# Optimization experiments

Measured on AMD Instinct MI355X. Metric: run time of the kernel, lower is better.

Reference implementation:

```python
import jax, jax.numpy as jnp
import numpy as np

GAMMA = 0.99      # discount_factor
LAM = 0.95        # gae_decay
CLIP = 0.2        # clipping_param
LOG_2PI = float(np.log(2.0 * np.pi))

B, T, A = 512, 2048, 16


def setup_inputs() -> dict:
    key = jax.random.key(0)
    ks = jax.random.split(key, 8)
    rewards = jax.random.normal(ks[0], (B, T), dtype=jnp.float32)
    critic_out = jax.random.normal(ks[1], (B, T + 1), dtype=jnp.float32)
    mu = jax.random.normal(ks[2], (B, T, A), dtype=jnp.float32)
    sigma = jax.random.uniform(ks[3], (B, T, A), dtype=jnp.float32) * 0.5 + 0.5
    old_mu = jax.random.normal(ks[4], (B, T, A), dtype=jnp.float32)
    old_sigma = jax.random.uniform(ks[5], (B, T, A), dtype=jnp.float32) * 0.5 + 0.5
    actions = jax.random.normal(ks[6], (B, T, A), dtype=jnp.float32)
    dones = jax.random.randint(ks[7], (B, T), 0, 2, dtype=jnp.int32)
    return {"rewards": rewards, "critic_out": critic_out, "mu": mu, "sigma": sigma,
            "old_mu": old_mu, "old_sigma": old_sigma, "actions": actions, "dones": dones}


def _normal_log_prob(x, mu, sigma):
    return -jnp.log(sigma) - 0.5 * LOG_2PI - 0.5 * jnp.square((x - mu) / sigma)


def _gae(rewards, dones_f, critic_out):
    # td_residuals: rewards + gamma * V[1:] - V[:-1]   -> [B, T]
    td = rewards + GAMMA * critic_out[:, 1:] - critic_out[:, :-1]
    b, t = rewards.shape
    # Reversed recurrence: adv[t] = td[t] + gamma*lam*(1 - done[t+1]) * adv[t+1],
    # for t = T-2 .. 0; adv[T-1] stays 0 (matches original loop bounds).
    xs = (jnp.flip(td[:, : t - 1], axis=1).T,        # [T-1, B]
          jnp.flip(dones_f[:, 1:], axis=1).T)        # [T-1, B]

    def step(carry, x):
        td_t, d_t = x
        adv = td_t + GAMMA * LAM * (1.0 - d_t) * carry
        return adv, adv

    _, advs = jax.lax.scan(step, jnp.zeros((b,), rewards.dtype), xs)
    advs = jnp.flip(advs, axis=0).T                  # [B, T-1]
    return jnp.concatenate([advs, jnp.zeros((b, 1), rewards.dtype)], axis=1)


def reference(rewards, critic_out, mu, sigma, old_mu, old_sigma, actions, dones):
    dones_f = dones.astype(rewards.dtype)
    advantages = _gae(rewards, dones_f, critic_out)          # [B, T]
    lp = _normal_log_prob(actions, mu, sigma)                # [B, T, A]
    old_lp = _normal_log_prob(actions, old_mu, old_sigma)    # [B, T, A]
    ratio = jnp.exp(lp - old_lp)
    clipped = jnp.minimum(jnp.maximum(ratio, 1.0 + CLIP), 1.0 - CLIP)
    adv = advantages[..., None]                              # broadcast over action dim
    obj = jnp.minimum(adv * ratio, adv * clipped)
    entropy = jnp.log(sigma) + 0.5 + 0.5 * LOG_2PI           # Normal entropy, [B, T, A]
    return jnp.mean(obj) + entropy
```

## Files before the change

### kernel.cpp

```cpp
#include <hip/hip_runtime.h>
#include <math.h>

#define BB 512
#define TT 2048
#define AA 16
#define NTOT (512LL * 2048LL * 16LL)
#define GAMMA 0.99f
#define GLAM  0.9405f
#define ENTC  1.4189385332046727f

#define NB2 2048

__global__ __launch_bounds__(256) void gae_kernel(
    const float* __restrict__ rewards, const float* __restrict__ vout,
    const int* __restrict__ dones, float* __restrict__ adv)
{
    const int b   = blockIdx.x;
    const int tid = threadIdx.x;
    const float* rw = rewards + (size_t)b * TT;
    const float* V  = vout    + (size_t)b * (TT + 1);
    const int*   dn = dones   + (size_t)b * TT;
    float*       av = adv     + (size_t)b * TT;

    float ak[8], bk[8];
    float SA = 1.f, SB = 0.f;
    #pragma unroll
    for (int k = 0; k < 8; ++k) {
        int u = tid * 8 + k;
        float au, bu;
        if (u == 0) { au = 0.f; bu = 0.f; }
        else {
            int t = TT - 1 - u;
            bu = rw[t] + GAMMA * V[t + 1] - V[t];
            au = GLAM * (1.f - (float)dn[t + 1]);
        }
        ak[k] = au; bk[k] = bu;
        SB = au * SB + bu;
        SA = au * SA;
    }

    const int lane = tid & 63;
    const int wave = tid >> 6;

    #pragma unroll
    for (int off = 1; off < 64; off <<= 1) {
        float pA = __shfl_up(SA, off, 64);
        float pB = __shfl_up(SB, off, 64);
        if (lane >= off) { SB = SA * pB + SB; SA = SA * pA; }
    }

    __shared__ float wA[4], wB[4];
    if (lane == 63) { wA[wave] = SA; wB[wave] = SB; }
    __syncthreads();

    float PA = 1.f, PB = 0.f;
    for (int w = 0; w < wave; ++w) {
        float aw = wA[w], bw = wB[w];
        PB = aw * PB + bw;
        PA = aw * PA;
    }

    float EA = __shfl_up(SA, 1, 64);
    float EB = __shfl_up(SB, 1, 64);
    if (lane == 0) { EA = 1.f; EB = 0.f; }

    float x = EA * PB + EB;
    #pragma unroll
    for (int k = 0; k < 8; ++k) {
        x = ak[k] * x + bk[k];
        int u = tid * 8 + k;
        av[TT - 1 - u] = x;
    }
}

__device__ __forceinline__ float obj1(float x, float m, float s,
                                      float om, float os, float ad)
{
    float rs  = __builtin_amdgcn_rcpf(s);
    float ros = __builtin_amdgcn_rcpf(os);
    float z   = (x - m) * rs;
    float zo  = (x - om) * ros;
    float d   = 0.5f * (zo * zo - z * z);
    float ratio = os * rs * __expf(d);
    return fminf(ad * ratio, ad * 0.8f);
}

__global__ __launch_bounds__(256) void obj_kernel(
    const float* __restrict__ mu, const float* __restrict__ sigma,
    const float* __restrict__ old_mu, const float* __restrict__ old_sigma,
    const float* __restrict__ actions, const float* __restrict__ adv,
    double* __restrict__ partials)
{
    const int tid = threadIdx.x;
    const size_t gthread = (size_t)blockIdx.x * 256 + tid;
    const size_t stride  = (size_t)NB2 * 256;

    const float4* m4  = (const float4*)mu;
    const float4* s4  = (const float4*)sigma;
    const float4* om4 = (const float4*)old_mu;
    const float4* os4 = (const float4*)old_sigma;
    const float4* x4  = (const float4*)actions;

    double lsum = 0.0;
    #pragma unroll 2
    for (int it = 0; it < 8; ++it) {
        size_t v = gthread + (size_t)it * stride;
        float4 m  = m4[v];
        float4 s  = s4[v];
        float4 om = om4[v];
        float4 os = os4[v];
        float4 x  = x4[v];
        float ad  = adv[v >> 2];

        float o0 = obj1(x.x, m.x, s.x, om.x, os.x, ad);
        float o1 = obj1(x.y, m.y, s.y, om.y, os.y, ad);
        float o2 = obj1(x.z, m.z, s.z, om.z, os.z, ad);
        float o3 = obj1(x.w, m.w, s.w, om.w, os.w, ad);
        lsum += (double)o0 + (double)o1 + (double)o2 + (double)o3;
    }

    #pragma unroll
    for (int off = 32; off > 0; off >>= 1)
        lsum += __shfl_down(lsum, off, 64);

    __shared__ double wsum[4];
    const int lane = tid & 63, wave = tid >> 6;
    if (lane == 0) wsum[wave] = lsum;
    __syncthreads();
    if (tid == 0)
        partials[blockIdx.x] = wsum[0] + wsum[1] + wsum[2] + wsum[3];
}

__global__ __launch_bounds__(256) void reduce_kernel(
    const double* __restrict__ partials, float* __restrict__ meanOut)
{
    const int tid = threadIdx.x;
    double s = 0.0;
    for (int i = tid; i < NB2; i += 256) s += partials[i];
    #pragma unroll
    for (int off = 32; off > 0; off >>= 1)
        s += __shfl_down(s, off, 64);
    __shared__ double wsum[4];
    const int lane = tid & 63, wave = tid >> 6;
    if (lane == 0) wsum[wave] = s;
    __syncthreads();
    if (tid == 0) {
        double total = wsum[0] + wsum[1] + wsum[2] + wsum[3];
        meanOut[0] = (float)(total / (double)NTOT);
    }
}

__global__ __launch_bounds__(256) void out_kernel(
    const float* __restrict__ sigma, const float* __restrict__ meanPtr,
    float* __restrict__ out)
{
    const size_t v = (size_t)blockIdx.x * 256 + threadIdx.x;
    const float mean = *meanPtr;
    float4 s = ((const float4*)sigma)[v];
    float4 o;
    o.x = mean + __logf(s.x) + ENTC;
    o.y = mean + __logf(s.y) + ENTC;
    o.z = mean + __logf(s.z) + ENTC;
    o.w = mean + __logf(s.w) + ENTC;
    ((float4*)out)[v] = o;
}

extern "C" void kernel_launch(void* const* d_in, const int* in_sizes, int n_in,
                              void* d_out, int out_size, void* d_ws, size_t ws_size,
                              hipStream_t stream) {
    const float* rewards   = (const float*)d_in[0];
    const float* critic    = (const float*)d_in[1];
    const float* mu        = (const float*)d_in[2];
    const float* sigma     = (const float*)d_in[3];
    const float* old_mu    = (const float*)d_in[4];
    const float* old_sigma = (const float*)d_in[5];
    const float* actions   = (const float*)d_in[6];
    const int*   dones     = (const int*)d_in[7];
    float* out = (float*)d_out;

    char* ws = (char*)d_ws;
    float*  meanPtr  = (float*)ws;
    double* partials = (double*)(ws + 256);
    float*  adv      = (float*)(ws + 32768);

    gae_kernel<<<BB, 256, 0, stream>>>(rewards, critic, dones, adv);
    obj_kernel<<<NB2, 256, 0, stream>>>(mu, sigma, old_mu, old_sigma,
                                        actions, adv, partials);
    reduce_kernel<<<1, 256, 0, stream>>>(partials, meanPtr);
    out_kernel<<<(int)(NTOT / 4 / 256), 256, 0, stream>>>(sigma, meanPtr, out);
}
```

Baseline: 344.5 us.

## Vectorize GAE loads, atomic-accumulate mean, drop reduce kernel, nontemporal streaming loads

```diff
diff --git a/kernel.cpp b/kernel.cpp
--- a/kernel.cpp
+++ b/kernel.cpp
@@ -10,30 +10,46 @@
 #define ENTC  1.4189385332046727f
 
 #define NB2 2048
+#define NB3 2048
+
+typedef float f32x4 __attribute__((ext_vector_type(4)));
 
 __global__ __launch_bounds__(256) void gae_kernel(
     const float* __restrict__ rewards, const float* __restrict__ vout,
-    const int* __restrict__ dones, float* __restrict__ adv)
+    const int* __restrict__ dones, float* __restrict__ adv,
+    double* __restrict__ total)
 {
     const int b   = blockIdx.x;
     const int tid = threadIdx.x;
+    if (b == 0 && tid == 0) *total = 0.0;
+
     const float* rw = rewards + (size_t)b * TT;
     const float* V  = vout    + (size_t)b * (TT + 1);
     const int*   dn = dones   + (size_t)b * TT;
     float*       av = adv     + (size_t)b * TT;
 
+    const int t_lo = TT - 8 - 8 * tid;
+
+    float4 rA = *(const float4*)(rw + t_lo);
+    float4 rB = *(const float4*)(rw + t_lo + 4);
+    int4   dA = *(const int4*)(dn + t_lo);
+    int4   dB = *(const int4*)(dn + t_lo + 4);
+    int    d8 = (tid == 0) ? 1 : dn[t_lo + 8];
+    float vv[9];
+    #pragma unroll
+    for (int j = 0; j < 9; ++j) vv[j] = V[t_lo + j];
+
+    float rr[8] = {rA.x, rA.y, rA.z, rA.w, rB.x, rB.y, rB.z, rB.w};
+    int   dd[9] = {dA.x, dA.y, dA.z, dA.w, dB.x, dB.y, dB.z, dB.w, d8};
+
     float ak[8], bk[8];
     float SA = 1.f, SB = 0.f;
     #pragma unroll
     for (int k = 0; k < 8; ++k) {
-        int u = tid * 8 + k;
-        float au, bu;
-        if (u == 0) { au = 0.f; bu = 0.f; }
-        else {
-            int t = TT - 1 - u;
-            bu = rw[t] + GAMMA * V[t + 1] - V[t];
-            au = GLAM * (1.f - (float)dn[t + 1]);
-        }
+        const int j = 7 - k;
+        float bu = rr[j] + GAMMA * vv[j + 1] - vv[j];
+        float au = GLAM * (1.f - (float)dd[j + 1]);
+        if (k == 0 && tid == 0) { au = 0.f; bu = 0.f; }
         ak[k] = au; bk[k] = bu;
         SB = au * SB + bu;
         SA = au * SA;
@@ -65,12 +81,14 @@
     if (lane == 0) { EA = 1.f; EB = 0.f; }
 
     float x = EA * PB + EB;
+    float outb[8];
     #pragma unroll
     for (int k = 0; k < 8; ++k) {
         x = ak[k] * x + bk[k];
-        int u = tid * 8 + k;
-        av[TT - 1 - u] = x;
-    }
+        outb[7 - k] = x;
+    }
+    *(float4*)(av + t_lo)     = make_float4(outb[0], outb[1], outb[2], outb[3]);
+    *(float4*)(av + t_lo + 4) = make_float4(outb[4], outb[5], outb[6], outb[7]);
 }
 
 __device__ __forceinline__ float obj1(float x, float m, float s,
@@ -85,39 +103,55 @@
     return fminf(ad * ratio, ad * 0.8f);
 }
 
+__device__ __forceinline__ double obj4d(f32x4 m, f32x4 s, f32x4 om, f32x4 os,
+                                        f32x4 x, float ad)
+{
+    float o0 = obj1(x.x, m.x, s.x, om.x, os.x, ad);
+    float o1 = obj1(x.y, m.y, s.y, om.y, os.y, ad);
+    float o2 = obj1(x.z, m.z, s.z, om.z, os.z, ad);
+    float o3 = obj1(x.w, m.w, s.w, om.w, os.w, ad);
+    return (double)o0 + (double)o1 + (double)o2 + (double)o3;
+}
+
 __global__ __launch_bounds__(256) void obj_kernel(
     const float* __restrict__ mu, const float* __restrict__ sigma,
     const float* __restrict__ old_mu, const float* __restrict__ old_sigma,
     const float* __restrict__ actions, const float* __restrict__ adv,
-    double* __restrict__ partials)
+    double* __restrict__ total)
 {
     const int tid = threadIdx.x;
-    const size_t gthread = (size_t)blockIdx.x * 256 + tid;
-    const size_t stride  = (size_t)NB2 * 256;
-
-    const float4* m4  = (const float4*)mu;
-    const float4* s4  = (const float4*)sigma;
-    const float4* om4 = (const float4*)old_mu;
-    const float4* os4 = (const float4*)old_sigma;
-    const float4* x4  = (const float4*)actions;
+    uint32_t v = (uint32_t)blockIdx.x * 256u + (uint32_t)tid;
+    const uint32_t stride = (uint32_t)NB2 * 256u;
+
+    const f32x4* m4  = (const f32x4*)mu;
+    const f32x4* s4  = (const f32x4*)sigma;
+    const f32x4* om4 = (const f32x4*)old_mu;
+    const f32x4* os4 = (const f32x4*)old_sigma;
+    const f32x4* x4  = (const f32x4*)actions;
+
+    f32x4 m0  = __builtin_nontemporal_load(m4 + v);
+    f32x4 s0  = s4[v];
+    f32x4 om0 = __builtin_nontemporal_load(om4 + v);
+    f32x4 os0 = __builtin_nontemporal_load(os4 + v);
+    f32x4 x0  = __builtin_nontemporal_load(x4 + v);
+    float a0  = adv[v >> 2];
 
     double lsum = 0.0;
-    #pragma unroll 2
-    for (int it = 0; it < 8; ++it) {
-        size_t v = gthread + (size_t)it * stride;
-        float4 m  = m4[v];
-        float4 s  = s4[v];
-        float4 om = om4[v];
-        float4 os = os4[v];
-        float4 x  = x4[v];
-        float ad  = adv[v >> 2];
-
-        float o0 = obj1(x.x, m.x, s.x, om.x, os.x, ad);
-        float o1 = obj1(x.y, m.y, s.y, om.y, os.y, ad);
-        float o2 = obj1(x.z, m.z, s.z, om.z, os.z, ad);
-        float o3 = obj1(x.w, m.w, s.w, om.w, os.w, ad);
-        lsum += (double)o0 + (double)o1 + (double)o2 + (double)o3;
-    }
+    #pragma unroll 1
+    for (int it = 0; it < 7; ++it) {
+        const uint32_t w = v + stride;
+        f32x4 m1  = __builtin_nontemporal_load(m4 + w);
+        f32x4 s1  = s4[w];
+        f32x4 om1 = __builtin_nontemporal_load(om4 + w);
+        f32x4 os1 = __builtin_nontemporal_load(os4 + w);
+        f32x4 x1  = __builtin_nontemporal_load(x4 + w);
+        float a1  = adv[w >> 2];
+
+        lsum += obj4d(m0, s0, om0, os0, x0, a0);
+
+        m0 = m1; s0 = s1; om0 = om1; os0 = os1; x0 = x1; a0 = a1; v = w;
+    }
+    lsum += obj4d(m0, s0, om0, os0, x0, a0);
 
     #pragma unroll
     for (int off = 32; off > 0; off >>= 1)
@@ -127,42 +161,44 @@
     const int lane = tid & 63, wave = tid >> 6;
     if (lane == 0) wsum[wave] = lsum;
     __syncthreads();
-    if (tid == 0)
-        partials[blockIdx.x] = wsum[0] + wsum[1] + wsum[2] + wsum[3];
-}
-
-__global__ __launch_bounds__(256) void reduce_kernel(
-    const double* __restrict__ partials, float* __restrict__ meanOut)
+    if (tid == 0) {
+        double bsum = wsum[0] + wsum[1] + wsum[2] + wsum[3];
+        __hip_atomic_fetch_add(total, bsum, __ATOMIC_RELAXED,
+                               __HIP_MEMORY_SCOPE_AGENT);
+    }
+}
+
+__global__ __launch_bounds__(256) void out_kernel(
+    const float* __restrict__ sigma, const double* __restrict__ total,
+    float* __restrict__ out)
 {
     const int tid = threadIdx.x;
-    double s = 0.0;
-    for (int i = tid; i < NB2; i += 256) s += partials[i];
-    #pragma unroll
-    for (int off = 32; off > 0; off >>= 1)
-        s += __shfl_down(s, off, 64);
-    __shared__ double wsum[4];
-    const int lane = tid & 63, wave = tid >> 6;
-    if (lane == 0) wsum[wave] = s;
-    __syncthreads();
-    if (tid == 0) {
-        double total = wsum[0] + wsum[1] + wsum[2] + wsum[3];
-        meanOut[0] = (float)(total / (double)NTOT);
-    }
-}
-
-__global__ __launch_bounds__(256) void out_kernel(
-    const float* __restrict__ sigma, const float* __restrict__ meanPtr,
-    float* __restrict__ out)
-{
-    const size_t v = (size_t)blockIdx.x * 256 + threadIdx.x;
-    const float mean = *meanPtr;
-    float4 s = ((const float4*)sigma)[v];
-    float4 o;
-    o.x = mean + __logf(s.x) + ENTC;
-    o.y = mean + __logf(s.y) + ENTC;
-    o.z = mean + __logf(s.z) + ENTC;
-    o.w = mean + __logf(s.w) + ENTC;
-    ((float4*)out)[v] = o;
+    const float mean = (float)(*total / (double)NTOT);
+
+    uint32_t v = (uint32_t)blockIdx.x * 256u + (uint32_t)tid;
+    const uint32_t stride = (uint32_t)NB3 * 256u;
+    const f32x4* s4 = (const f32x4*)sigma;
+    f32x4* o4 = (f32x4*)out;
+
+    f32x4 s0 = s4[v];
+    #pragma unroll 1
+    for (int it = 0; it < 7; ++it) {
+        const uint32_t w = v + stride;
+        f32x4 s1 = s4[w];
+        f32x4 o;
+        o.x = mean + __logf(s0.x) + ENTC;
+        o.y = mean + __logf(s0.y) + ENTC;
+        o.z = mean + __logf(s0.z) + ENTC;
+        o.w = mean + __logf(s0.w) + ENTC;
+        __builtin_nontemporal_store(o, o4 + v);
+        s0 = s1; v = w;
+    }
+    f32x4 o;
+    o.x = mean + __logf(s0.x) + ENTC;
+    o.y = mean + __logf(s0.y) + ENTC;
+    o.z = mean + __logf(s0.z) + ENTC;
+    o.w = mean + __logf(s0.w) + ENTC;
+    __builtin_nontemporal_store(o, o4 + v);
 }
 
 extern "C" void kernel_launch(void* const* d_in, const int* in_sizes, int n_in,
@@ -179,13 +215,11 @@
     float* out = (float*)d_out;
 
     char* ws = (char*)d_ws;
-    float*  meanPtr  = (float*)ws;
-    double* partials = (double*)(ws + 256);
-    float*  adv      = (float*)(ws + 32768);
-
-    gae_kernel<<<BB, 256, 0, stream>>>(rewards, critic, dones, adv);
+    double* total = (double*)ws;
+    float*  adv   = (float*)(ws + 32768);
+
+    gae_kernel<<<BB, 256, 0, stream>>>(rewards, critic, dones, adv, total);
     obj_kernel<<<NB2, 256, 0, stream>>>(mu, sigma, old_mu, old_sigma,
-                                        actions, adv, partials);
-    reduce_kernel<<<1, 256, 0, stream>>>(partials, meanPtr);
-    out_kernel<<<(int)(NTOT / 4 / 256), 256, 0, stream>>>(sigma, meanPtr, out);
-}
+                                        actions, adv, total);
+    out_kernel<<<NB3, 256, 0, stream>>>(sigma, total, out);
+}
```

New measurement: 322.9 us. -6.3%, faster.

## Fuse GAE scan into objective kernel and fold reduction into output pass

Applied to the files above, without the earlier changes.

```diff
diff --git a/kernel.cpp b/kernel.cpp
--- a/kernel.cpp
+++ b/kernel.cpp
@@ -9,69 +9,9 @@
 #define GLAM  0.9405f
 #define ENTC  1.4189385332046727f
 
-#define NB2 2048
-
-__global__ __launch_bounds__(256) void gae_kernel(
-    const float* __restrict__ rewards, const float* __restrict__ vout,
-    const int* __restrict__ dones, float* __restrict__ adv)
-{
-    const int b   = blockIdx.x;
-    const int tid = threadIdx.x;
-    const float* rw = rewards + (size_t)b * TT;
-    const float* V  = vout    + (size_t)b * (TT + 1);
-    const int*   dn = dones   + (size_t)b * TT;
-    float*       av = adv     + (size_t)b * TT;
-
-    float ak[8], bk[8];
-    float SA = 1.f, SB = 0.f;
-    #pragma unroll
-    for (int k = 0; k < 8; ++k) {
-        int u = tid * 8 + k;
-        float au, bu;
-        if (u == 0) { au = 0.f; bu = 0.f; }
-        else {
-            int t = TT - 1 - u;
-            bu = rw[t] + GAMMA * V[t + 1] - V[t];
-            au = GLAM * (1.f - (float)dn[t + 1]);
-        }
-        ak[k] = au; bk[k] = bu;
-        SB = au * SB + bu;
-        SA = au * SA;
-    }
-
-    const int lane = tid & 63;
-    const int wave = tid >> 6;
-
-    #pragma unroll
-    for (int off = 1; off < 64; off <<= 1) {
-        float pA = __shfl_up(SA, off, 64);
-        float pB = __shfl_up(SB, off, 64);
-        if (lane >= off) { SB = SA * pB + SB; SA = SA * pA; }
-    }
-
-    __shared__ float wA[4], wB[4];
-    if (lane == 63) { wA[wave] = SA; wB[wave] = SB; }
-    __syncthreads();
-
-    float PA = 1.f, PB = 0.f;
-    for (int w = 0; w < wave; ++w) {
-        float aw = wA[w], bw = wB[w];
-        PB = aw * PB + bw;
-        PA = aw * PA;
-    }
-
-    float EA = __shfl_up(SA, 1, 64);
-    float EB = __shfl_up(SB, 1, 64);
-    if (lane == 0) { EA = 1.f; EB = 0.f; }
-
-    float x = EA * PB + EB;
-    #pragma unroll
-    for (int k = 0; k < 8; ++k) {
-        x = ak[k] * x + bk[k];
-        int u = tid * 8 + k;
-        av[TT - 1 - u] = x;
-    }
-}
+#define NB3 2048
+
+typedef float f32x4 __attribute__((ext_vector_type(4)));
 
 __device__ __forceinline__ float obj1(float x, float m, float s,
                                       float om, float os, float ad)
@@ -85,84 +25,192 @@
     return fminf(ad * ratio, ad * 0.8f);
 }
 
-__global__ __launch_bounds__(256) void obj_kernel(
+__device__ __forceinline__ double obj4d(f32x4 m, f32x4 s, f32x4 om, f32x4 os,
+                                        f32x4 x, float ad)
+{
+    float o0 = obj1(x.x, m.x, s.x, om.x, os.x, ad);
+    float o1 = obj1(x.y, m.y, s.y, om.y, os.y, ad);
+    float o2 = obj1(x.z, m.z, s.z, om.z, os.z, ad);
+    float o3 = obj1(x.w, m.w, s.w, om.w, os.w, ad);
+    return (double)o0 + (double)o1 + (double)o2 + (double)o3;
+}
+
+__global__ __launch_bounds__(512, 4) void gae_obj_kernel(
+    const float* __restrict__ rewards, const float* __restrict__ vout,
+    const int* __restrict__ dones,
     const float* __restrict__ mu, const float* __restrict__ sigma,
     const float* __restrict__ old_mu, const float* __restrict__ old_sigma,
-    const float* __restrict__ actions, const float* __restrict__ adv,
+    const float* __restrict__ actions,
     double* __restrict__ partials)
 {
-    const int tid = threadIdx.x;
-    const size_t gthread = (size_t)blockIdx.x * 256 + tid;
-    const size_t stride  = (size_t)NB2 * 256;
-
-    const float4* m4  = (const float4*)mu;
-    const float4* s4  = (const float4*)sigma;
-    const float4* om4 = (const float4*)old_mu;
-    const float4* os4 = (const float4*)old_sigma;
-    const float4* x4  = (const float4*)actions;
+    __shared__ float  adv_s[TT];
+    __shared__ float  wA[8], wB[8];
+    __shared__ double wsum[8];
+
+    const int b    = blockIdx.x;
+    const int tid  = threadIdx.x;
+    const int lane = tid & 63;
+    const int wave = tid >> 6;
+
+    {
+        const float* rw = rewards + (size_t)b * TT;
+        const float* V  = vout    + (size_t)b * (TT + 1);
+        const int*   dn = dones   + (size_t)b * TT;
+
+        const int t_lo = TT - 4 - 4 * tid;
+
+        f32x4 r4 = *(const f32x4*)(rw + t_lo);
+        int4  d4 = *(const int4*)(dn + t_lo);
+        int   dt = (tid == 0) ? 1 : dn[t_lo + 4];
+        float vv[5];
+        #pragma unroll
+        for (int j = 0; j < 5; ++j) vv[j] = V[t_lo + j];
+
+        float rr[4] = {r4.x, r4.y, r4.z, r4.w};
+        int   dd[5] = {d4.x, d4.y, d4.z, d4.w, dt};
+
+        float ak[4], bk[4];
+        float SA = 1.f, SB = 0.f;
+        #pragma unroll
+        for (int k = 0; k < 4; ++k) {
+            const int j = 3 - k;
+            float bu = rr[j] + GAMMA * vv[j + 1] - vv[j];
+            float au = GLAM * (1.f - (float)dd[j + 1]);
+            if (k == 0 && tid == 0) { au = 0.f; bu = 0.f; }
+            ak[k] = au; bk[k] = bu;
+            SB = au * SB + bu;
+            SA = au * SA;
+        }
+
+        #pragma unroll
+        for (int off = 1; off < 64; off <<= 1) {
+            float pA = __shfl_up(SA, off, 64);
+            float pB = __shfl_up(SB, off, 64);
+            if (lane >= off) { SB = SA * pB + SB; SA = SA * pA; }
+        }
+
+        if (lane == 63) { wA[wave] = SA; wB[wave] = SB; }
+        __syncthreads();
+
+        float PA = 1.f, PB = 0.f;
+        for (int w = 0; w < wave; ++w) {
+            float aw = wA[w], bw = wB[w];
+            PB = aw * PB + bw;
+            PA = aw * PA;
+        }
+
+        float EA = __shfl_up(SA, 1, 64);
+        float EB = __shfl_up(SB, 1, 64);
+        if (lane == 0) { EA = 1.f; EB = 0.f; }
+
+        float x = EA * PB + EB;
+        float outb[4];
+        #pragma unroll
+        for (int k = 0; k < 4; ++k) {
+            x = ak[k] * x + bk[k];
+            outb[3 - k] = x;
+        }
+        *(f32x4*)(adv_s + t_lo) = (f32x4){outb[0], outb[1], outb[2], outb[3]};
+    }
+    __syncthreads();
+
+    const size_t rowf4 = (size_t)b * (TT * AA / 4);
+    const f32x4* m4  = (const f32x4*)mu        + rowf4;
+    const f32x4* s4  = (const f32x4*)sigma     + rowf4;
+    const f32x4* om4 = (const f32x4*)old_mu    + rowf4;
+    const f32x4* os4 = (const f32x4*)old_sigma + rowf4;
+    const f32x4* x4  = (const f32x4*)actions   + rowf4;
+
+    uint32_t f = (uint32_t)tid;
+    f32x4 m0  = __builtin_nontemporal_load(m4 + f);
+    f32x4 s0  = s4[f];
+    f32x4 om0 = __builtin_nontemporal_load(om4 + f);
+    f32x4 os0 = __builtin_nontemporal_load(os4 + f);
+    f32x4 x0  = __builtin_nontemporal_load(x4 + f);
+    float a0  = adv_s[f >> 2];
 
     double lsum = 0.0;
-    #pragma unroll 2
-    for (int it = 0; it < 8; ++it) {
-        size_t v = gthread + (size_t)it * stride;
-        float4 m  = m4[v];
-        float4 s  = s4[v];
-        float4 om = om4[v];
-        float4 os = os4[v];
-        float4 x  = x4[v];
-        float ad  = adv[v >> 2];
-
-        float o0 = obj1(x.x, m.x, s.x, om.x, os.x, ad);
-        float o1 = obj1(x.y, m.y, s.y, om.y, os.y, ad);
-        float o2 = obj1(x.z, m.z, s.z, om.z, os.z, ad);
-        float o3 = obj1(x.w, m.w, s.w, om.w, os.w, ad);
-        lsum += (double)o0 + (double)o1 + (double)o2 + (double)o3;
-    }
+    #pragma unroll 1
+    for (int it = 0; it < 15; ++it) {
+        const uint32_t fn = f + 512u;
+        f32x4 m1  = __builtin_nontemporal_load(m4 + fn);
+        f32x4 s1  = s4[fn];
+        f32x4 om1 = __builtin_nontemporal_load(om4 + fn);
+        f32x4 os1 = __builtin_nontemporal_load(os4 + fn);
+        f32x4 x1  = __builtin_nontemporal_load(x4 + fn);
+        float a1  = adv_s[fn >> 2];
+
+        lsum += obj4d(m0, s0, om0, os0, x0, a0);
+
+        m0 = m1; s0 = s1; om0 = om1; os0 = os1; x0 = x1; a0 = a1; f = fn;
+    }
+    lsum += obj4d(m0, s0, om0, os0, x0, a0);
 
     #pragma unroll
     for (int off = 32; off > 0; off >>= 1)
         lsum += __shfl_down(lsum, off, 64);
-
-    __shared__ double wsum[4];
+    if (lane == 0) wsum[wave] = lsum;
+    __syncthreads();
+    if (tid == 0) {
+        double t = 0.0;
+        #pragma unroll
+        for (int w = 0; w < 8; ++w) t += wsum[w];
+        partials[b] = t;
+    }
+}
+
+__global__ __launch_bounds__(256) void out_kernel(
+    const float* __restrict__ sigma, const double* __restrict__ partials,
+    float* __restrict__ out)
+{
+    const int tid  = threadIdx.x;
     const int lane = tid & 63, wave = tid >> 6;
-    if (lane == 0) wsum[wave] = lsum;
-    __syncthreads();
-    if (tid == 0)
-        partials[blockIdx.x] = wsum[0] + wsum[1] + wsum[2] + wsum[3];
-}
-
-__global__ __launch_bounds__(256) void reduce_kernel(
-    const double* __restrict__ partials, float* __restrict__ meanOut)
-{
-    const int tid = threadIdx.x;
-    double s = 0.0;
-    for (int i = tid; i < NB2; i += 256) s += partials[i];
+
+    double s = partials[tid] + partials[tid + 256];
     #pragma unroll
     for (int off = 32; off > 0; off >>= 1)
         s += __shfl_down(s, off, 64);
     __shared__ double wsum[4];
-    const int lane = tid & 63, wave = tid >> 6;
+    __shared__ float  mean_s;
     if (lane == 0) wsum[wave] = s;
     __syncthreads();
-    if (tid == 0) {
-        double total = wsum[0] + wsum[1] + wsum[2] + wsum[3];
-        meanOut[0] = (float)(total / (double)NTOT);
-    }
-}
-
-__global__ __launch_bounds__(256) void out_kernel(
-    const float* __restrict__ sigma, const float* __restrict__ meanPtr,
-    float* __restrict__ out)
-{
-    const size_t v = (size_t)blockIdx.x * 256 + threadIdx.x;
-    const float mean = *meanPtr;
-    float4 s = ((const float4*)sigma)[v];
-    float4 o;
-    o.x = mean + __logf(s.x) + ENTC;
-    o.y = mean + __logf(s.y) + ENTC;
-    o.z = mean + __logf(s.z) + ENTC;
-    o.w = mean + __logf(s.w) + ENTC;
-    ((float4*)out)[v] = o;
+    if (tid == 0)
+        mean_s = (float)((wsum[0] + wsum[1] + wsum[2] + wsum[3]) / (double)NTOT);
+    __syncthreads();
+    const float mean = mean_s;
+
+    const uint32_t HALF = (uint32_t)(NTOT / 4 / 2);
+    const uint32_t STEP = (uint32_t)NB3 * 256u;
+    uint32_t v = (uint32_t)blockIdx.x * 256u + (uint32_t)tid;
+
+    const f32x4* s4 = (const f32x4*)sigma;
+    f32x4* o4 = (f32x4*)out;
+
+    f32x4 a0 = s4[v];
+    f32x4 b0 = s4[v + HALF];
+    #pragma unroll 1
+    for (int it = 0; it < 3; ++it) {
+        const uint32_t vn = v + STEP;
+        f32x4 a1 = s4[vn];
+        f32x4 b1 = s4[vn + HALF];
+
+        f32x4 oa, ob;
+        oa.x = mean + __logf(a0.x) + ENTC;  oa.y = mean + __logf(a0.y) + ENTC;
+        oa.z = mean + __logf(a0.z) + ENTC;  oa.w = mean + __logf(a0.w) + ENTC;
+        ob.x = mean + __logf(b0.x) + ENTC;  ob.y = mean + __logf(b0.y) + ENTC;
+        ob.z = mean + __logf(b0.z) + ENTC;  ob.w = mean + __logf(b0.w) + ENTC;
+        __builtin_nontemporal_store(oa, o4 + v);
+        __builtin_nontemporal_store(ob, o4 + v + HALF);
+
+        a0 = a1; b0 = b1; v = vn;
+    }
+    f32x4 oa, ob;
+    oa.x = mean + __logf(a0.x) + ENTC;  oa.y = mean + __logf(a0.y) + ENTC;
+    oa.z = mean + __logf(a0.z) + ENTC;  oa.w = mean + __logf(a0.w) + ENTC;
+    ob.x = mean + __logf(b0.x) + ENTC;  ob.y = mean + __logf(b0.y) + ENTC;
+    ob.z = mean + __logf(b0.z) + ENTC;  ob.w = mean + __logf(b0.w) + ENTC;
+    __builtin_nontemporal_store(oa, o4 + v);
+    __builtin_nontemporal_store(ob, o4 + v + HALF);
 }
 
 extern "C" void kernel_launch(void* const* d_in, const int* in_sizes, int n_in,
@@ -178,14 +226,10 @@
     const int*   dones     = (const int*)d_in[7];
     float* out = (float*)d_out;
 
-    char* ws = (char*)d_ws;
-    float*  meanPtr  = (float*)ws;
-    double* partials = (double*)(ws + 256);
-    float*  adv      = (float*)(ws + 32768);
-
-    gae_kernel<<<BB, 256, 0, stream>>>(rewards, critic, dones, adv);
-    obj_kernel<<<NB2, 256, 0, stream>>>(mu, sigma, old_mu, old_sigma,
-                                        actions, adv, partials);
-    reduce_kernel<<<1, 256, 0, stream>>>(partials, meanPtr);
-    out_kernel<<<(int)(NTOT / 4 / 256), 256, 0, stream>>>(sigma, meanPtr, out);
-}
+    double* partials = (double*)d_ws;
+
+    gae_obj_kernel<<<BB, 512, 0, stream>>>(rewards, critic, dones,
+                                           mu, sigma, old_mu, old_sigma,
+                                           actions, partials);
+    out_kernel<<<NB3, 256, 0, stream>>>(sigma, partials, out);
+}
```

Result: faster. 324.7 us (-5.8%).
